# Kernel optimization log

Measured on AMD Instinct MI355X. Metric: run time of the kernel, lower is better.

Reference implementation:

```python
import jax, jax.numpy as jnp
import numpy as np

B, T, I, H, O, P = 32, 8192, 16, 128, 3, 1024


def setup_inputs() -> dict:
    key = jax.random.key(0)
    ks = jax.random.split(key, 8)
    x = jax.random.normal(ks[0], (B, T, I), dtype=jnp.float32)
    # feature channel 2 holds the photo id (original code does x[:,:,2].long())
    ids = jax.random.randint(ks[1], (B, T), 0, P)
    x = x.at[:, :, 2].set(ids.astype(jnp.float32))
    s = 1.0 / np.sqrt(H).astype(np.float32)
    W_ih = jax.random.uniform(ks[2], (4 * H, I), minval=-s, maxval=s, dtype=jnp.float32)
    W_hh = jax.random.uniform(ks[3], (4 * H, H), minval=-s, maxval=s, dtype=jnp.float32)
    b_ih = jax.random.uniform(ks[4], (4 * H,), minval=-s, maxval=s, dtype=jnp.float32)
    b_hh = jax.random.uniform(ks[5], (4 * H,), minval=-s, maxval=s, dtype=jnp.float32)
    W_fc = jax.random.uniform(ks[6], (O, H), minval=-s, maxval=s, dtype=jnp.float32)
    b_fc = jax.random.uniform(ks[7], (O,), minval=-s, maxval=s, dtype=jnp.float32)
    return dict(x=x, W_ih=W_ih, W_hh=W_hh, b_ih=b_ih, b_hh=b_hh,
                W_fc=W_fc, b_fc=b_fc, num_photos=P)


def _lstm(x, W_ih, W_hh, b_ih, b_hh):
    # single-layer batch_first LSTM, PyTorch gate order (i, f, g, o), zero init state
    Bz = x.shape[0]
    Hh = W_hh.shape[1]
    # precompute input contribution for all timesteps: [B, T, 4H]
    xg = jnp.einsum('bti,gi->btg', x, W_ih) + b_ih + b_hh

    def step(carry, gx):
        h, c = carry
        g = gx + h @ W_hh.T
        i, f, gg, o = jnp.split(g, 4, axis=-1)
        i = jax.nn.sigmoid(i)
        f = jax.nn.sigmoid(f)
        gg = jnp.tanh(gg)
        o = jax.nn.sigmoid(o)
        c = f * c + i * gg
        h = o * jnp.tanh(c)
        return (h, c), h

    h0 = jnp.zeros((Bz, Hh), x.dtype)
    _, hs = jax.lax.scan(step, (h0, h0), jnp.swapaxes(xg, 0, 1))  # [T, B, H]
    return jnp.swapaxes(hs, 0, 1)  # [B, T, H]


def reference(x, W_ih, W_hh, b_ih, b_hh, W_fc, b_fc, num_photos):
    Bz, T, _ = x.shape
    h = _lstm(x, W_ih, W_hh, b_ih, b_hh)          # [B, T, H]
    out = h @ W_fc.T + b_fc                        # [B, T, 3]
    ids = x[:, :, 2].astype(jnp.int32)             # [B, T]
    valid = ids < num_photos
    safe = jnp.where(valid, ids, 0)
    # flatten (batch, photo_id) into a single segment id per element
    seg = (jnp.arange(Bz, dtype=jnp.int32)[:, None] * num_photos + safe).reshape(-1)
    w = valid.astype(out.dtype)
    sums = jax.ops.segment_sum((out * w[..., None]).reshape(-1, out.shape[-1]),
                               seg, num_segments=Bz * num_photos)
    sums = sums.reshape(Bz, num_photos, out.shape[-1])
    counts = jax.ops.segment_sum(w.reshape(-1), seg, num_segments=Bz * num_photos)
    counts = counts.reshape(Bz, num_photos, 1)
    counts = jnp.where(counts == 0, 1.0, counts)   # matches photo_counts[photo_counts==0]=1
    return sums / counts
```

## Files before the change

### kernel.cpp

```cpp
#include <hip/hip_runtime.h>

#define B_ 32
#define T_ 8192
#define I_ 16
#define H_ 128
#define P_ 1024
#define O_ 3

typedef _Float16 h2 __attribute__((ext_vector_type(2)));
typedef _Float16 h4 __attribute__((ext_vector_type(4)));
typedef _Float16 h8 __attribute__((ext_vector_type(8)));

#if __has_builtin(__builtin_amdgcn_fdot2)
#define FDOT2(a, b, c) __builtin_amdgcn_fdot2((a), (b), (c), false)
#else
__device__ __forceinline__ float fdot2_asm(h2 a, h2 b, float c) {
    asm("v_dot2_f32_f16 %0, %1, %2, %0" : "+v"(c) : "v"(a), "v"(b));
    return c;
}
#define FDOT2(a, b, c) fdot2_asm((a), (b), (c))
#endif

#define FORME(M, g) M(g,0,0) M(g,0,1) M(g,0,2) M(g,0,3) \
                    M(g,1,0) M(g,1,1) M(g,1,2) M(g,1,3) \
                    M(g,2,0) M(g,2,1) M(g,2,2) M(g,2,3) \
                    M(g,3,0) M(g,3,1) M(g,3,2) M(g,3,3)
#define FORALL(M) FORME(M,0) FORME(M,1) FORME(M,2) FORME(M,3)
#define FORG(M) M(0) M(1) M(2) M(3)

#define DPPF(v, ctrl) \
    __int_as_float(__builtin_amdgcn_mov_dpp(__float_as_int(v), (ctrl), 0xF, 0xF, true))

__device__ __forceinline__ float xor32_add(float p) {
    float a = p, b = p;
    asm("v_permlane32_swap_b32 %0, %1" : "+v"(a), "+v"(b));
    return a + b;
}

__device__ __forceinline__ float tanh_f(float x) {
    return 2.f / (1.f + __expf(-2.f * x)) - 1.f;
}
__device__ __forceinline__ h4 cvt4(float4 v) {
    return (h4){(_Float16)v.x, (_Float16)v.y, (_Float16)v.z, (_Float16)v.w};
}

__device__ __forceinline__ void lds_barrier() {
    asm volatile("s_waitcnt lgkmcnt(0)\n\ts_barrier" ::: "memory");
}

__global__ __launch_bounds__(256, 1) __attribute__((amdgpu_waves_per_eu(1, 1)))
void lstm_fused(
    const float* __restrict__ x,
    const float* __restrict__ W_ih,
    const float* __restrict__ W_hh,
    const float* __restrict__ b_ih,
    const float* __restrict__ b_hh,
    const float* __restrict__ W_fc,
    float* __restrict__ sums,
    float* __restrict__ counts)
{
    const int b   = blockIdx.x;
    const int tid = threadIdx.x;
    const int q   = tid >> 2;
    const int kc  = tid & 3;
    const int ja  = 2 * q;
    const int jb  = 2 * q + 1;

    __shared__ __align__(16) _Float16 hh[2][H_];
    __shared__ __align__(16) _Float16 xt[2][16 * I_];
    __shared__ float sums_lds[P_ * O_];
    __shared__ float counts_lds[P_];

    const float* wrA0 = W_hh + (0 * H_ + ja) * H_;
    const float* wrA1 = W_hh + (1 * H_ + ja) * H_;
    const float* wrA2 = W_hh + (2 * H_ + ja) * H_;
    const float* wrA3 = W_hh + (3 * H_ + ja) * H_;
    const float* wrB0 = W_hh + (0 * H_ + jb) * H_;
    const float* wrB1 = W_hh + (1 * H_ + jb) * H_;
    const float* wrB2 = W_hh + (2 * H_ + jb) * H_;
    const float* wrB3 = W_hh + (3 * H_ + jb) * H_;
    #define WLOADA(g, m, e) h2 WA##g##_##m##_##e = (h2){ \
        (_Float16)wrA##g[kc * 8 + 32 * (m) + 2 * (e)], \
        (_Float16)wrA##g[kc * 8 + 32 * (m) + 2 * (e) + 1]};
    #define WLOADB(g, m, e) h2 WB##g##_##m##_##e = (h2){ \
        (_Float16)wrB##g[kc * 8 + 32 * (m) + 2 * (e)], \
        (_Float16)wrB##g[kc * 8 + 32 * (m) + 2 * (e) + 1]};
    FORALL(WLOADA)
    FORALL(WLOADB)

    #define ULOADA(g) \
        h2 UA##g##_0 = (h2){(_Float16)W_ih[((g) * H_ + ja) * I_ + kc * 4 + 0], \
                            (_Float16)W_ih[((g) * H_ + ja) * I_ + kc * 4 + 1]}; \
        h2 UA##g##_1 = (h2){(_Float16)W_ih[((g) * H_ + ja) * I_ + kc * 4 + 2], \
                            (_Float16)W_ih[((g) * H_ + ja) * I_ + kc * 4 + 3]};
    #define ULOADB(g) \
        h2 UB##g##_0 = (h2){(_Float16)W_ih[((g) * H_ + jb) * I_ + kc * 4 + 0], \
                            (_Float16)W_ih[((g) * H_ + jb) * I_ + kc * 4 + 1]}; \
        h2 UB##g##_1 = (h2){(_Float16)W_ih[((g) * H_ + jb) * I_ + kc * 4 + 2], \
                            (_Float16)W_ih[((g) * H_ + jb) * I_ + kc * 4 + 3]};
    FORG(ULOADA)
    FORG(ULOADB)

    const float biasA = b_ih[kc * H_ + ja] + b_hh[kc * H_ + ja];
    const float biasB = b_ih[kc * H_ + jb] + b_hh[kc * H_ + jb];
    const float wfcA  = (kc < 3) ? W_fc[kc * H_ + ja] : 0.f;
    const float wfcB  = (kc < 3) ? W_fc[kc * H_ + jb] : 0.f;

    const bool fc_lane = ((tid & 0x2C) == 0) && (kc < 3);

    for (int i = tid; i < P_ * O_; i += 256) sums_lds[i] = 0.f;
    for (int i = tid; i < P_;      i += 256) counts_lds[i] = 0.f;
    if (tid < H_) hh[0][tid] = (_Float16)0.f;

    const float* xb = x + (size_t)b * T_ * I_;
    float4 xr4 = make_float4(0.f, 0.f, 0.f, 0.f);
    if (tid < 64) {
        xr4 = ((const float4*)xb)[tid];
        *(h4*)&xt[0][tid * 4] = cvt4(xr4);
    }
    float cA = 0.f, cB = 0.f;
    float pend_p = 0.f;
    int   pend_id = 0;
    __syncthreads();

    #pragma unroll 1
    for (int t = 0; t < T_; ++t) {
        const int off = t & 15;
        const int btx = (t >> 4) & 1;
        const int bh  = t & 1;

        if (t != 0) {
            if (fc_lane && (unsigned)pend_id < (unsigned)P_)
                atomicAdd(&sums_lds[pend_id * O_ + kc], pend_p);
            if (tid == 0 && (unsigned)pend_id < (unsigned)P_)
                atomicAdd(&counts_lds[pend_id], 1.f);
        }

        if (tid < 64) {
            if (off == 0 && t + 16 < T_)
                xr4 = ((const float4*)(xb + (t + 16) * I_))[tid];
            if (off == 8 && t + 8 < T_)
                *(h4*)&xt[btx ^ 1][tid * 4] = cvt4(xr4);
        }

        const h4 xv4 = *(const h4*)&xt[btx][off * I_ + kc * 4];
        const h2 xv0 = __builtin_shufflevector(xv4, xv4, 0, 1);
        const h2 xv1 = __builtin_shufflevector(xv4, xv4, 2, 3);
        const int id = (int)(float)xt[btx][off * I_ + 2];

        float aA0 = 0.f, aA1 = 0.f, aA2 = 0.f, aA3 = 0.f;
        float aB0 = 0.f, aB1 = 0.f, aB2 = 0.f, aB3 = 0.f;
        #define HD(m) { \
            h8 hv = *(const h8*)&hh[bh][kc * 8 + 32 * (m)]; \
            h2 p0 = __builtin_shufflevector(hv, hv, 0, 1); \
            h2 p1 = __builtin_shufflevector(hv, hv, 2, 3); \
            h2 p2 = __builtin_shufflevector(hv, hv, 4, 5); \
            h2 p3 = __builtin_shufflevector(hv, hv, 6, 7); \
            aA0 = FDOT2(p0, WA0_##m##_0, aA0); aA0 = FDOT2(p1, WA0_##m##_1, aA0); \
            aA0 = FDOT2(p2, WA0_##m##_2, aA0); aA0 = FDOT2(p3, WA0_##m##_3, aA0); \
            aA1 = FDOT2(p0, WA1_##m##_0, aA1); aA1 = FDOT2(p1, WA1_##m##_1, aA1); \
            aA1 = FDOT2(p2, WA1_##m##_2, aA1); aA1 = FDOT2(p3, WA1_##m##_3, aA1); \
            aA2 = FDOT2(p0, WA2_##m##_0, aA2); aA2 = FDOT2(p1, WA2_##m##_1, aA2); \
            aA2 = FDOT2(p2, WA2_##m##_2, aA2); aA2 = FDOT2(p3, WA2_##m##_3, aA2); \
            aA3 = FDOT2(p0, WA3_##m##_0, aA3); aA3 = FDOT2(p1, WA3_##m##_1, aA3); \
            aA3 = FDOT2(p2, WA3_##m##_2, aA3); aA3 = FDOT2(p3, WA3_##m##_3, aA3); \
            aB0 = FDOT2(p0, WB0_##m##_0, aB0); aB0 = FDOT2(p1, WB0_##m##_1, aB0); \
            aB0 = FDOT2(p2, WB0_##m##_2, aB0); aB0 = FDOT2(p3, WB0_##m##_3, aB0); \
            aB1 = FDOT2(p0, WB1_##m##_0, aB1); aB1 = FDOT2(p1, WB1_##m##_1, aB1); \
            aB1 = FDOT2(p2, WB1_##m##_2, aB1); aB1 = FDOT2(p3, WB1_##m##_3, aB1); \
            aB2 = FDOT2(p0, WB2_##m##_0, aB2); aB2 = FDOT2(p1, WB2_##m##_1, aB2); \
            aB2 = FDOT2(p2, WB2_##m##_2, aB2); aB2 = FDOT2(p3, WB2_##m##_3, aB2); \
            aB3 = FDOT2(p0, WB3_##m##_0, aB3); aB3 = FDOT2(p1, WB3_##m##_1, aB3); \
            aB3 = FDOT2(p2, WB3_##m##_2, aB3); aB3 = FDOT2(p3, WB3_##m##_3, aB3); }
        HD(0) HD(1) HD(2) HD(3)
        aA0 = FDOT2(xv0, UA0_0, aA0); aA0 = FDOT2(xv1, UA0_1, aA0);
        aA1 = FDOT2(xv0, UA1_0, aA1); aA1 = FDOT2(xv1, UA1_1, aA1);
        aA2 = FDOT2(xv0, UA2_0, aA2); aA2 = FDOT2(xv1, UA2_1, aA2);
        aA3 = FDOT2(xv0, UA3_0, aA3); aA3 = FDOT2(xv1, UA3_1, aA3);
        aB0 = FDOT2(xv0, UB0_0, aB0); aB0 = FDOT2(xv1, UB0_1, aB0);
        aB1 = FDOT2(xv0, UB1_0, aB1); aB1 = FDOT2(xv1, UB1_1, aB1);
        aB2 = FDOT2(xv0, UB2_0, aB2); aB2 = FDOT2(xv1, UB2_1, aB2);
        aB3 = FDOT2(xv0, UB3_0, aB3); aB3 = FDOT2(xv1, UB3_1, aB3);

        float s_;
        s_ = DPPF(aA0, 0xB1); aA0 += s_;
        s_ = DPPF(aA1, 0xB1); aA1 += s_;
        s_ = DPPF(aA2, 0xB1); aA2 += s_;
        s_ = DPPF(aA3, 0xB1); aA3 += s_;
        s_ = DPPF(aB0, 0xB1); aB0 += s_;
        s_ = DPPF(aB1, 0xB1); aB1 += s_;
        s_ = DPPF(aB2, 0xB1); aB2 += s_;
        s_ = DPPF(aB3, 0xB1); aB3 += s_;
        s_ = DPPF(aA0, 0x4E); aA0 += s_;
        s_ = DPPF(aA1, 0x4E); aA1 += s_;
        s_ = DPPF(aA2, 0x4E); aA2 += s_;
        s_ = DPPF(aA3, 0x4E); aA3 += s_;
        s_ = DPPF(aB0, 0x4E); aB0 += s_;
        s_ = DPPF(aB1, 0x4E); aB1 += s_;
        s_ = DPPF(aB2, 0x4E); aB2 += s_;
        s_ = DPPF(aB3, 0x4E); aB3 += s_;

        float tgA = (kc == 0) ? aA0 : (kc == 1) ? aA1 : (kc == 2) ? aA2 : aA3;
        float tgB = (kc == 0) ? aB0 : (kc == 1) ? aB1 : (kc == 2) ? aB2 : aB3;
        tgA += biasA;
        tgB += biasB;
        const bool  isg  = (kc == 2);
        const float argA = isg ? (tgA + tgA) : tgA;
        const float argB = isg ? (tgB + tgB) : tgB;
        const float sfA  = 1.f / (1.f + __expf(-argA));
        const float sfB  = 1.f / (1.f + __expf(-argB));
        const float actA = isg ? (sfA + sfA - 1.f) : sfA;
        const float actB = isg ? (sfB + sfB - 1.f) : sfB;

        const float giA = DPPF(actA, 0x00);
        const float gfA = DPPF(actA, 0x55);
        const float ggA = DPPF(actA, 0xAA);
        const float goA = DPPF(actA, 0xFF);
        const float giB = DPPF(actB, 0x00);
        const float gfB = DPPF(actB, 0x55);
        const float ggB = DPPF(actB, 0xAA);
        const float goB = DPPF(actB, 0xFF);
        cA = fmaf(gfA, cA, giA * ggA);
        cB = fmaf(gfB, cB, giB * ggB);
        const float hnA = goA * tanh_f(cA);
        const float hnB = goB * tanh_f(cB);

        if (kc == 0) {
            h2 hp = (h2){(_Float16)hnA, (_Float16)hnB};
            *(h2*)&hh[bh ^ 1][ja] = hp;
        }

        float p = fmaf(hnA, wfcA, hnB * wfcB);
        p += DPPF(p, 0x124);
        p += DPPF(p, 0x128);
        p = xor32_add(p);
        pend_p  = p;
        pend_id = id;

        lds_barrier();
    }

    if (fc_lane && (unsigned)pend_id < (unsigned)P_)
        atomicAdd(&sums_lds[pend_id * O_ + kc], pend_p);
    if (tid == 0 && (unsigned)pend_id < (unsigned)P_)
        atomicAdd(&counts_lds[pend_id], 1.f);
    __syncthreads();

    float* sums_g = sums + (size_t)b * P_ * O_;
    for (int i = tid; i < P_ * O_; i += 256) sums_g[i] = sums_lds[i];
    float* cnt_g = counts + (size_t)b * P_;
    for (int i = tid; i < P_; i += 256) cnt_g[i] = counts_lds[i];
}

__global__ void finalize_kernel(const float* __restrict__ sums,
                                const float* __restrict__ counts,
                                const float* __restrict__ b_fc,
                                float* __restrict__ out)
{
    const int idx = blockIdx.x * blockDim.x + threadIdx.x;
    if (idx >= B_ * P_ * O_) return;
    const int o  = idx % O_;
    const int bp = idx / O_;
    const float cnt = counts[bp];
    const float denom = (cnt > 0.f) ? cnt : 1.f;
    out[idx] = (sums[idx] + cnt * b_fc[o]) / denom;
}

extern "C" void kernel_launch(void* const* d_in, const int* in_sizes, int n_in,
                              void* d_out, int out_size, void* d_ws, size_t ws_size,
                              hipStream_t stream) {
    const float* x    = (const float*)d_in[0];
    const float* W_ih = (const float*)d_in[1];
    const float* W_hh = (const float*)d_in[2];
    const float* b_ih = (const float*)d_in[3];
    const float* b_hh = (const float*)d_in[4];
    const float* W_fc = (const float*)d_in[5];
    const float* b_fc = (const float*)d_in[6];

    float* out    = (float*)d_out;
    float* sums   = (float*)d_ws;
    float* counts = sums + (size_t)B_ * P_ * O_;

    lstm_fused<<<B_, 256, 0, stream>>>(x, W_ih, W_hh, b_ih, b_hh, W_fc, sums, counts);

    const int n = B_ * P_ * O_;
    finalize_kernel<<<(n + 255) / 256, 256, 0, stream>>>(sums, counts, b_fc, out);
}
```

Before: 6.057 ms.

## Process two batch sequences per block sharing register-resident weights

Each block now runs the LSTM recurrence for two batch rows at once, reusing the same register-held W_hh/W_ih fragments, and halves the grid to B/2 blocks. It aims to amortize per-step barrier, LDS and reduction latency over twice the independent work and to give more instruction-level parallelism. In exchange each step does twice the dot-product work on half as many CUs, and per-block LDS and register pressure increase.

After: 10.58 ms. +74.7%, slower.

```diff
diff --git a/kernel.cpp b/kernel.cpp
--- a/kernel.cpp
+++ b/kernel.cpp
@@ -59,17 +59,19 @@
     float* __restrict__ sums,
     float* __restrict__ counts)
 {
-    const int b   = blockIdx.x;
+    const int bx  = blockIdx.x;
+    const int b0  = 2 * bx;
+    const int b1  = 2 * bx + 1;
     const int tid = threadIdx.x;
     const int q   = tid >> 2;
     const int kc  = tid & 3;
     const int ja  = 2 * q;
     const int jb  = 2 * q + 1;
 
-    __shared__ __align__(16) _Float16 hh[2][H_];
-    __shared__ __align__(16) _Float16 xt[2][16 * I_];
-    __shared__ float sums_lds[P_ * O_];
-    __shared__ float counts_lds[P_];
+    __shared__ __align__(16) _Float16 hh[2][2][H_];
+    __shared__ __align__(16) _Float16 xt[2][2][16 * I_];
+    __shared__ float sums_lds[2][P_ * O_];
+    __shared__ float counts_lds[2][P_];
 
     const float* wrA0 = W_hh + (0 * H_ + ja) * H_;
     const float* wrA1 = W_hh + (1 * H_ + ja) * H_;
@@ -105,22 +107,34 @@
     const float biasB = b_ih[kc * H_ + jb] + b_hh[kc * H_ + jb];
     const float wfcA  = (kc < 3) ? W_fc[kc * H_ + ja] : 0.f;
     const float wfcB  = (kc < 3) ? W_fc[kc * H_ + jb] : 0.f;
+    const bool  isg   = (kc == 2);
 
     const bool fc_lane = ((tid & 0x2C) == 0) && (kc < 3);
 
-    for (int i = tid; i < P_ * O_; i += 256) sums_lds[i] = 0.f;
-    for (int i = tid; i < P_;      i += 256) counts_lds[i] = 0.f;
-    if (tid < H_) hh[0][tid] = (_Float16)0.f;
-
-    const float* xb = x + (size_t)b * T_ * I_;
-    float4 xr4 = make_float4(0.f, 0.f, 0.f, 0.f);
+    for (int i = tid; i < P_ * O_; i += 256) {
+        sums_lds[0][i] = 0.f; sums_lds[1][i] = 0.f;
+    }
+    for (int i = tid; i < P_; i += 256) {
+        counts_lds[0][i] = 0.f; counts_lds[1][i] = 0.f;
+    }
+    if (tid < H_) {
+        hh[0][0][tid] = (_Float16)0.f;
+        hh[1][0][tid] = (_Float16)0.f;
+    }
+
+    const float* xb0 = x + (size_t)b0 * T_ * I_;
+    const float* xb1 = x + (size_t)b1 * T_ * I_;
+    float4 xr4_0 = make_float4(0.f, 0.f, 0.f, 0.f);
+    float4 xr4_1 = make_float4(0.f, 0.f, 0.f, 0.f);
     if (tid < 64) {
-        xr4 = ((const float4*)xb)[tid];
-        *(h4*)&xt[0][tid * 4] = cvt4(xr4);
-    }
-    float cA = 0.f, cB = 0.f;
-    float pend_p = 0.f;
-    int   pend_id = 0;
+        xr4_0 = ((const float4*)xb0)[tid];
+        xr4_1 = ((const float4*)xb1)[tid];
+        *(h4*)&xt[0][0][tid * 4] = cvt4(xr4_0);
+        *(h4*)&xt[1][0][tid * 4] = cvt4(xr4_1);
+    }
+    float cA_0 = 0.f, cB_0 = 0.f, cA_1 = 0.f, cB_1 = 0.f;
+    float pend_p0 = 0.f, pend_p1 = 0.f;
+    int   pend_id0 = 0, pend_id1 = 0;
     __syncthreads();
 
     #pragma unroll 1
@@ -130,126 +144,153 @@
         const int bh  = t & 1;
 
         if (t != 0) {
-            if (fc_lane && (unsigned)pend_id < (unsigned)P_)
-                atomicAdd(&sums_lds[pend_id * O_ + kc], pend_p);
-            if (tid == 0 && (unsigned)pend_id < (unsigned)P_)
-                atomicAdd(&counts_lds[pend_id], 1.f);
+            if (fc_lane) {
+                if ((unsigned)pend_id0 < (unsigned)P_)
+                    atomicAdd(&sums_lds[0][pend_id0 * O_ + kc], pend_p0);
+                if ((unsigned)pend_id1 < (unsigned)P_)
+                    atomicAdd(&sums_lds[1][pend_id1 * O_ + kc], pend_p1);
+            }
+            if (tid == 0) {
+                if ((unsigned)pend_id0 < (unsigned)P_)
+                    atomicAdd(&counts_lds[0][pend_id0], 1.f);
+                if ((unsigned)pend_id1 < (unsigned)P_)
+                    atomicAdd(&counts_lds[1][pend_id1], 1.f);
+            }
         }
 
         if (tid < 64) {
-            if (off == 0 && t + 16 < T_)
-                xr4 = ((const float4*)(xb + (t + 16) * I_))[tid];
-            if (off == 8 && t + 8 < T_)
-                *(h4*)&xt[btx ^ 1][tid * 4] = cvt4(xr4);
+            if (off == 0 && t + 16 < T_) {
+                xr4_0 = ((const float4*)(xb0 + (t + 16) * I_))[tid];
+                xr4_1 = ((const float4*)(xb1 + (t + 16) * I_))[tid];
+            }
+            if (off == 8 && t + 8 < T_) {
+                *(h4*)&xt[0][btx ^ 1][tid * 4] = cvt4(xr4_0);
+                *(h4*)&xt[1][btx ^ 1][tid * 4] = cvt4(xr4_1);
+            }
         }
 
-        const h4 xv4 = *(const h4*)&xt[btx][off * I_ + kc * 4];
-        const h2 xv0 = __builtin_shufflevector(xv4, xv4, 0, 1);
-        const h2 xv1 = __builtin_shufflevector(xv4, xv4, 2, 3);
-        const int id = (int)(float)xt[btx][off * I_ + 2];
-
-        float aA0 = 0.f, aA1 = 0.f, aA2 = 0.f, aA3 = 0.f;
-        float aB0 = 0.f, aB1 = 0.f, aB2 = 0.f, aB3 = 0.f;
-        #define HD(m) { \
-            h8 hv = *(const h8*)&hh[bh][kc * 8 + 32 * (m)]; \
+        const h4 xv4_0 = *(const h4*)&xt[0][btx][off * I_ + kc * 4];
+        const h4 xv4_1 = *(const h4*)&xt[1][btx][off * I_ + kc * 4];
+        const h2 xv0_0 = __builtin_shufflevector(xv4_0, xv4_0, 0, 1);
+        const h2 xv1_0 = __builtin_shufflevector(xv4_0, xv4_0, 2, 3);
+        const h2 xv0_1 = __builtin_shufflevector(xv4_1, xv4_1, 0, 1);
+        const h2 xv1_1 = __builtin_shufflevector(xv4_1, xv4_1, 2, 3);
+        const int id0 = (int)(float)xt[0][btx][off * I_ + 2];
+        const int id1 = (int)(float)xt[1][btx][off * I_ + 2];
+
+        float aA0_0 = 0.f, aA1_0 = 0.f, aA2_0 = 0.f, aA3_0 = 0.f;
+        float aB0_0 = 0.f, aB1_0 = 0.f, aB2_0 = 0.f, aB3_0 = 0.f;
+        float aA0_1 = 0.f, aA1_1 = 0.f, aA2_1 = 0.f, aA3_1 = 0.f;
+        float aB0_1 = 0.f, aB1_1 = 0.f, aB2_1 = 0.f, aB3_1 = 0.f;
+        #define HDX(X, m) { \
+            h8 hv = *(const h8*)&hh[X][bh][kc * 8 + 32 * (m)]; \
             h2 p0 = __builtin_shufflevector(hv, hv, 0, 1); \
             h2 p1 = __builtin_shufflevector(hv, hv, 2, 3); \
             h2 p2 = __builtin_shufflevector(hv, hv, 4, 5); \
             h2 p3 = __builtin_shufflevector(hv, hv, 6, 7); \
-            aA0 = FDOT2(p0, WA0_##m##_0, aA0); aA0 = FDOT2(p1, WA0_##m##_1, aA0); \
-            aA0 = FDOT2(p2, WA0_##m##_2, aA0); aA0 = FDOT2(p3, WA0_##m##_3, aA0); \
-            aA1 = FDOT2(p0, WA1_##m##_0, aA1); aA1 = FDOT2(p1, WA1_##m##_1, aA1); \
-            aA1 = FDOT2(p2, WA1_##m##_2, aA1); aA1 = FDOT2(p3, WA1_##m##_3, aA1); \
-            aA2 = FDOT2(p0, WA2_##m##_0, aA2); aA2 = FDOT2(p1, WA2_##m##_1, aA2); \
-            aA2 = FDOT2(p2, WA2_##m##_2, aA2); aA2 = FDOT2(p3, WA2_##m##_3, aA2); \
-            aA3 = FDOT2(p0, WA3_##m##_0, aA3); aA3 = FDOT2(p1, WA3_##m##_1, aA3); \
-            aA3 = FDOT2(p2, WA3_##m##_2, aA3); aA3 = FDOT2(p3, WA3_##m##_3, aA3); \
-            aB0 = FDOT2(p0, WB0_##m##_0, aB0); aB0 = FDOT2(p1, WB0_##m##_1, aB0); \
-            aB0 = FDOT2(p2, WB0_##m##_2, aB0); aB0 = FDOT2(p3, WB0_##m##_3, aB0); \
-            aB1 = FDOT2(p0, WB1_##m##_0, aB1); aB1 = FDOT2(p1, WB1_##m##_1, aB1); \
-            aB1 = FDOT2(p2, WB1_##m##_2, aB1); aB1 = FDOT2(p3, WB1_##m##_3, aB1); \
-            aB2 = FDOT2(p0, WB2_##m##_0, aB2); aB2 = FDOT2(p1, WB2_##m##_1, aB2); \
-            aB2 = FDOT2(p2, WB2_##m##_2, aB2); aB2 = FDOT2(p3, WB2_##m##_3, aB2); \
-            aB3 = FDOT2(p0, WB3_##m##_0, aB3); aB3 = FDOT2(p1, WB3_##m##_1, aB3); \
-            aB3 = FDOT2(p2, WB3_##m##_2, aB3); aB3 = FDOT2(p3, WB3_##m##_3, aB3); }
-        HD(0) HD(1) HD(2) HD(3)
-        aA0 = FDOT2(xv0, UA0_0, aA0); aA0 = FDOT2(xv1, UA0_1, aA0);
-        aA1 = FDOT2(xv0, UA1_0, aA1); aA1 = FDOT2(xv1, UA1_1, aA1);
-        aA2 = FDOT2(xv0, UA2_0, aA2); aA2 = FDOT2(xv1, UA2_1, aA2);
-        aA3 = FDOT2(xv0, UA3_0, aA3); aA3 = FDOT2(xv1, UA3_1, aA3);
-        aB0 = FDOT2(xv0, UB0_0, aB0); aB0 = FDOT2(xv1, UB0_1, aB0);
-        aB1 = FDOT2(xv0, UB1_0, aB1); aB1 = FDOT2(xv1, UB1_1, aB1);
-        aB2 = FDOT2(xv0, UB2_0, aB2); aB2 = FDOT2(xv1, UB2_1, aB2);
-        aB3 = FDOT2(xv0, UB3_0, aB3); aB3 = FDOT2(xv1, UB3_1, aB3);
-
-        float s_;
-        s_ = DPPF(aA0, 0xB1); aA0 += s_;
-        s_ = DPPF(aA1, 0xB1); aA1 += s_;
-        s_ = DPPF(aA2, 0xB1); aA2 += s_;
-        s_ = DPPF(aA3, 0xB1); aA3 += s_;
-        s_ = DPPF(aB0, 0xB1); aB0 += s_;
-        s_ = DPPF(aB1, 0xB1); aB1 += s_;
-        s_ = DPPF(aB2, 0xB1); aB2 += s_;
-        s_ = DPPF(aB3, 0xB1); aB3 += s_;
-        s_ = DPPF(aA0, 0x4E); aA0 += s_;
-        s_ = DPPF(aA1, 0x4E); aA1 += s_;
-        s_ = DPPF(aA2, 0x4E); aA2 += s_;
-        s_ = DPPF(aA3, 0x4E); aA3 += s_;
-        s_ = DPPF(aB0, 0x4E); aB0 += s_;
-        s_ = DPPF(aB1, 0x4E); aB1 += s_;
-        s_ = DPPF(aB2, 0x4E); aB2 += s_;
-        s_ = DPPF(aB3, 0x4E); aB3 += s_;
-
-        float tgA = (kc == 0) ? aA0 : (kc == 1) ? aA1 : (kc == 2) ? aA2 : aA3;
-        float tgB = (kc == 0) ? aB0 : (kc == 1) ? aB1 : (kc == 2) ? aB2 : aB3;
-        tgA += biasA;
-        tgB += biasB;
-        const bool  isg  = (kc == 2);
-        const float argA = isg ? (tgA + tgA) : tgA;
-        const float argB = isg ? (tgB + tgB) : tgB;
-        const float sfA  = 1.f / (1.f + __expf(-argA));
-        const float sfB  = 1.f / (1.f + __expf(-argB));
-        const float actA = isg ? (sfA + sfA - 1.f) : sfA;
-        const float actB = isg ? (sfB + sfB - 1.f) : sfB;
-
-        const float giA = DPPF(actA, 0x00);
-        const float gfA = DPPF(actA, 0x55);
-        const float ggA = DPPF(actA, 0xAA);
-        const float goA = DPPF(actA, 0xFF);
-        const float giB = DPPF(actB, 0x00);
-        const float gfB = DPPF(actB, 0x55);
-        const float ggB = DPPF(actB, 0xAA);
-        const float goB = DPPF(actB, 0xFF);
-        cA = fmaf(gfA, cA, giA * ggA);
-        cB = fmaf(gfB, cB, giB * ggB);
-        const float hnA = goA * tanh_f(cA);
-        const float hnB = goB * tanh_f(cB);
+            aA0_##X = FDOT2(p0, WA0_##m##_0, aA0_##X); aA0_##X = FDOT2(p1, WA0_##m##_1, aA0_##X); \
+            aA0_##X = FDOT2(p2, WA0_##m##_2, aA0_##X); aA0_##X = FDOT2(p3, WA0_##m##_3, aA0_##X); \
+            aA1_##X = FDOT2(p0, WA1_##m##_0, aA1_##X); aA1_##X = FDOT2(p1, WA1_##m##_1, aA1_##X); \
+            aA1_##X = FDOT2(p2, WA1_##m##_2, aA1_##X); aA1_##X = FDOT2(p3, WA1_##m##_3, aA1_##X); \
+            aA2_##X = FDOT2(p0, WA2_##m##_0, aA2_##X); aA2_##X = FDOT2(p1, WA2_##m##_1, aA2_##X); \
+            aA2_##X = FDOT2(p2, WA2_##m##_2, aA2_##X); aA2_##X = FDOT2(p3, WA2_##m##_3, aA2_##X); \
+            aA3_##X = FDOT2(p0, WA3_##m##_0, aA3_##X); aA3_##X = FDOT2(p1, WA3_##m##_1, aA3_##X); \
+            aA3_##X = FDOT2(p2, WA3_##m##_2, aA3_##X); aA3_##X = FDOT2(p3, WA3_##m##_3, aA3_##X); \
+            aB0_##X = FDOT2(p0, WB0_##m##_0, aB0_##X); aB0_##X = FDOT2(p1, WB0_##m##_1, aB0_##X); \
+            aB0_##X = FDOT2(p2, WB0_##m##_2, aB0_##X); aB0_##X = FDOT2(p3, WB0_##m##_3, aB0_##X); \
+            aB1_##X = FDOT2(p0, WB1_##m##_0, aB1_##X); aB1_##X = FDOT2(p1, WB1_##m##_1, aB1_##X); \
+            aB1_##X = FDOT2(p2, WB1_##m##_2, aB1_##X); aB1_##X = FDOT2(p3, WB1_##m##_3, aB1_##X); \
+            aB2_##X = FDOT2(p0, WB2_##m##_0, aB2_##X); aB2_##X = FDOT2(p1, WB2_##m##_1, aB2_##X); \
+            aB2_##X = FDOT2(p2, WB2_##m##_2, aB2_##X); aB2_##X = FDOT2(p3, WB2_##m##_3, aB2_##X); \
+            aB3_##X = FDOT2(p0, WB3_##m##_0, aB3_##X); aB3_##X = FDOT2(p1, WB3_##m##_1, aB3_##X); \
+            aB3_##X = FDOT2(p2, WB3_##m##_2, aB3_##X); aB3_##X = FDOT2(p3, WB3_##m##_3, aB3_##X); }
+        HDX(0, 0) HDX(0, 1) HDX(0, 2) HDX(0, 3)
+        HDX(1, 0) HDX(1, 1) HDX(1, 2) HDX(1, 3)
+        #define XC(X) \
+            aA0_##X = FDOT2(xv0_##X, UA0_0, aA0_##X); aA0_##X = FDOT2(xv1_##X, UA0_1, aA0_##X); \
+            aA1_##X = FDOT2(xv0_##X, UA1_0, aA1_##X); aA1_##X = FDOT2(xv1_##X, UA1_1, aA1_##X); \
+            aA2_##X = FDOT2(xv0_##X, UA2_0, aA2_##X); aA2_##X = FDOT2(xv1_##X, UA2_1, aA2_##X); \
+            aA3_##X = FDOT2(xv0_##X, UA3_0, aA3_##X); aA3_##X = FDOT2(xv1_##X, UA3_1, aA3_##X); \
+            aB0_##X = FDOT2(xv0_##X, UB0_0, aB0_##X); aB0_##X = FDOT2(xv1_##X, UB0_1, aB0_##X); \
+            aB1_##X = FDOT2(xv0_##X, UB1_0, aB1_##X); aB1_##X = FDOT2(xv1_##X, UB1_1, aB1_##X); \
+            aB2_##X = FDOT2(xv0_##X, UB2_0, aB2_##X); aB2_##X = FDOT2(xv1_##X, UB2_1, aB2_##X); \
+            aB3_##X = FDOT2(xv0_##X, UB3_0, aB3_##X); aB3_##X = FDOT2(xv1_##X, UB3_1, aB3_##X);
+        XC(0)
+        XC(1)
+
+        #define BFLY(ctrl, v) { float s_ = DPPF(v, ctrl); v += s_; }
+        BFLY(0xB1, aA0_0) BFLY(0xB1, aA1_0) BFLY(0xB1, aA2_0) BFLY(0xB1, aA3_0)
+        BFLY(0xB1, aB0_0) BFLY(0xB1, aB1_0) BFLY(0xB1, aB2_0) BFLY(0xB1, aB3_0)
+        BFLY(0xB1, aA0_1) BFLY(0xB1, aA1_1) BFLY(0xB1, aA2_1) BFLY(0xB1, aA3_1)
+        BFLY(0xB1, aB0_1) BFLY(0xB1, aB1_1) BFLY(0xB1, aB2_1) BFLY(0xB1, aB3_1)
+        BFLY(0x4E, aA0_0) BFLY(0x4E, aA1_0) BFLY(0x4E, aA2_0) BFLY(0x4E, aA3_0)
+        BFLY(0x4E, aB0_0) BFLY(0x4E, aB1_0) BFLY(0x4E, aB2_0) BFLY(0x4E, aB3_0)
+        BFLY(0x4E, aA0_1) BFLY(0x4E, aA1_1) BFLY(0x4E, aA2_1) BFLY(0x4E, aA3_1)
+        BFLY(0x4E, aB0_1) BFLY(0x4E, aB1_1) BFLY(0x4E, aB2_1) BFLY(0x4E, aB3_1)
+
+        #define ACT(X) \
+            float hnA_##X, hnB_##X; { \
+            float tgA = (kc == 0) ? aA0_##X : (kc == 1) ? aA1_##X : (kc == 2) ? aA2_##X : aA3_##X; \
+            float tgB = (kc == 0) ? aB0_##X : (kc == 1) ? aB1_##X : (kc == 2) ? aB2_##X : aB3_##X; \
+            tgA += biasA; tgB += biasB; \
+            const float argA = isg ? (tgA + tgA) : tgA; \
+            const float argB = isg ? (tgB + tgB) : tgB; \
+            const float sfA  = 1.f / (1.f + __expf(-argA)); \
+            const float sfB  = 1.f / (1.f + __expf(-argB)); \
+            const float actA = isg ? (sfA + sfA - 1.f) : sfA; \
+            const float actB = isg ? (sfB + sfB - 1.f) : sfB; \
+            const float giA = DPPF(actA, 0x00); const float gfA = DPPF(actA, 0x55); \
+            const float ggA = DPPF(actA, 0xAA); const float goA = DPPF(actA, 0xFF); \
+            const float giB = DPPF(actB, 0x00); const float gfB = DPPF(actB, 0x55); \
+            const float ggB = DPPF(actB, 0xAA); const float goB = DPPF(actB, 0xFF); \
+            cA_##X = fmaf(gfA, cA_##X, giA * ggA); \
+            cB_##X = fmaf(gfB, cB_##X, giB * ggB); \
+            hnA_##X = goA * tanh_f(cA_##X); \
+            hnB_##X = goB * tanh_f(cB_##X); }
+        ACT(0)
+        ACT(1)
 
         if (kc == 0) {
-            h2 hp = (h2){(_Float16)hnA, (_Float16)hnB};
-            *(h2*)&hh[bh ^ 1][ja] = hp;
+            *(h2*)&hh[0][bh ^ 1][ja] = (h2){(_Float16)hnA_0, (_Float16)hnB_0};
+            *(h2*)&hh[1][bh ^ 1][ja] = (h2){(_Float16)hnA_1, (_Float16)hnB_1};
         }
 
-        float p = fmaf(hnA, wfcA, hnB * wfcB);
-        p += DPPF(p, 0x124);
-        p += DPPF(p, 0x128);
-        p = xor32_add(p);
-        pend_p  = p;
-        pend_id = id;
+        float p0v = fmaf(hnA_0, wfcA, hnB_0 * wfcB);
+        p0v += DPPF(p0v, 0x124);
+        p0v += DPPF(p0v, 0x128);
+        p0v = xor32_add(p0v);
+        float p1v = fmaf(hnA_1, wfcA, hnB_1 * wfcB);
+        p1v += DPPF(p1v, 0x124);
+        p1v += DPPF(p1v, 0x128);
+        p1v = xor32_add(p1v);
+        pend_p0 = p0v; pend_id0 = id0;
+        pend_p1 = p1v; pend_id1 = id1;
 
         lds_barrier();
     }
 
-    if (fc_lane && (unsigned)pend_id < (unsigned)P_)
-        atomicAdd(&sums_lds[pend_id * O_ + kc], pend_p);
-    if (tid == 0 && (unsigned)pend_id < (unsigned)P_)
-        atomicAdd(&counts_lds[pend_id], 1.f);
+    if (fc_lane) {
+        if ((unsigned)pend_id0 < (unsigned)P_)
+            atomicAdd(&sums_lds[0][pend_id0 * O_ + kc], pend_p0);
+        if ((unsigned)pend_id1 < (unsigned)P_)
+            atomicAdd(&sums_lds[1][pend_id1 * O_ + kc], pend_p1);
+    }
+    if (tid == 0) {
+        if ((unsigned)pend_id0 < (unsigned)P_)
+            atomicAdd(&counts_lds[0][pend_id0], 1.f);
+        if ((unsigned)pend_id1 < (unsigned)P_)
+            atomicAdd(&counts_lds[1][pend_id1], 1.f);
+    }
     __syncthreads();
 
-    float* sums_g = sums + (size_t)b * P_ * O_;
-    for (int i = tid; i < P_ * O_; i += 256) sums_g[i] = sums_lds[i];
-    float* cnt_g = counts + (size_t)b * P_;
-    for (int i = tid; i < P_; i += 256) cnt_g[i] = counts_lds[i];
+    for (int i = tid; i < P_ * O_; i += 256) {
+        sums[(size_t)b0 * P_ * O_ + i] = sums_lds[0][i];
+        sums[(size_t)b1 * P_ * O_ + i] = sums_lds[1][i];
+    }
+    for (int i = tid; i < P_; i += 256) {
+        counts[(size_t)b0 * P_ + i] = counts_lds[0][i];
+        counts[(size_t)b1 * P_ + i] = counts_lds[1][i];
+    }
 }
 
 __global__ void finalize_kernel(const float* __restrict__ sums,
@@ -281,7 +322,8 @@
     float* sums   = (float*)d_ws;
     float* counts = sums + (size_t)B_ * P_ * O_;
 
-    lstm_fused<<<B_, 256, 0, stream>>>(x, W_ih, W_hh, b_ih, b_hh, W_fc, sums, counts);
+    lstm_fused<<<B_ / 2, 256, 0, stream>>>(x, W_ih, W_hh, b_ih, b_hh, W_fc,
+                                           sums, counts);
 
     const int n = B_ * P_ * O_;
     finalize_kernel<<<(n + 255) / 256, 256, 0, stream>>>(sums, counts, b_fc, out);
```
